# Kernel tuning notes

Hardware: AMD Instinct MI355X
Metric: run time of the kernel (lower is better)

Reference implementation:

```python
import jax, jax.numpy as jnp
import numpy as np

N = 200_000      # nodes
E = 6_400_000    # edges (avg degree 32)
ATT = 16         # scorer hidden dim
MAXD = 512       # mixer max_depth
C = 1.0          # curvature
EPS = 1e-15


def _mobius_add(a, b, c):
    # Mobius addition on the Poincare ball: a (+)_c b
    ab = jnp.sum(a * b, axis=-1, keepdims=True)
    aa = jnp.sum(a * a, axis=-1, keepdims=True)
    bb = jnp.sum(b * b, axis=-1, keepdims=True)
    num = (1.0 + 2.0 * c * ab + c * bb) * a + (1.0 - c * aa) * b
    den = 1.0 + 2.0 * c * ab + (c * c) * aa * bb
    return num / jnp.maximum(den, EPS)


def setup_inputs() -> dict:
    key = jax.random.key(0)
    ks = jax.random.split(key, 8)
    x = jax.random.normal(ks[0], (N, 2), dtype=jnp.float32)
    # keep nodes strictly inside the unit Poincare disk (|x| < 0.5)
    x = 0.5 * x / (1.0 + jnp.linalg.norm(x, axis=-1, keepdims=True))
    edge_index = jax.random.randint(ks[1], (2, E), 0, N, dtype=jnp.int32)
    depth = jax.random.randint(ks[2], (N,), 0, MAXD, dtype=jnp.int32)
    W1 = jax.random.normal(ks[3], (2, ATT), dtype=jnp.float32) * (1.0 / np.sqrt(2.0))
    b1 = jnp.zeros((ATT,), dtype=jnp.float32)
    W2 = jax.random.normal(ks[4], (ATT, 1), dtype=jnp.float32) * (1.0 / np.sqrt(ATT))
    eta = jnp.array(1.0, dtype=jnp.float32)
    depth_scale = 1.0 + 0.1 * jax.random.normal(ks[5], (MAXD, 1), dtype=jnp.float32)
    depth_theta = 0.1 * jax.random.normal(ks[6], (MAXD, 1), dtype=jnp.float32)
    return dict(x=x, edge_index=edge_index, depth=depth, W1=W1, b1=b1, W2=W2,
                eta=eta, depth_scale=depth_scale, depth_theta=depth_theta)


def reference(x, edge_index, depth, W1, b1, W2, eta, depth_scale, depth_theta):
    c = C
    sc = jnp.sqrt(jnp.asarray(c, dtype=x.dtype))
    row, col = edge_index[0], edge_index[1]
    xi = x[row]   # [E,2] target node of each edge
    xj = x[col]   # [E,2] source node of each edge

    # log_{xi}(xj): tangent vector at xi
    u = _mobius_add(-xi, xj, c)                                        # [E,2]
    un = jnp.maximum(jnp.linalg.norm(u, axis=-1, keepdims=True), EPS)  # [E,1]
    lam_i = 2.0 / jnp.maximum(1.0 - c * jnp.sum(xi * xi, axis=-1, keepdims=True), EPS)
    v = (2.0 / (sc * lam_i)) * jnp.arctanh(jnp.minimum(sc * un, 1.0 - 1e-5)) * (u / un)

    # tiny MLP attention score per edge
    h = jax.nn.gelu(v @ W1 + b1, approximate=False)   # [E,ATT]
    scores = (h @ W2)[:, 0]                           # [E]

    # segment softmax over edges grouped by target node `row`
    smax = jax.ops.segment_max(scores, row, num_segments=N)
    ex = jnp.exp(scores - smax[row])
    denom = jax.ops.segment_sum(ex, row, num_segments=N)
    alpha = ex / jnp.maximum(denom[row], 1e-15)       # [E]

    # weighted scatter-add of tangent vectors
    m = jax.ops.segment_sum(alpha[:, None] * v, row, num_segments=N)   # [N,2]

    # depth-gated rotation/scale in the tangent space (mixer)
    d = jnp.clip(depth, 0, MAXD - 1)
    k = depth_scale[d]            # [N,1]
    ang = depth_theta[d][:, 0]    # [N]
    ca, sa = jnp.cos(ang), jnp.sin(ang)
    m = k * jnp.stack([ca * m[:, 0] - sa * m[:, 1],
                       sa * m[:, 0] + ca * m[:, 1]], axis=-1)

    # exp_{x}(eta * m)
    w = eta * m
    wn = jnp.maximum(jnp.linalg.norm(w, axis=-1, keepdims=True), EPS)
    lam_x = 2.0 / jnp.maximum(1.0 - c * jnp.sum(x * x, axis=-1, keepdims=True), EPS)
    second = jnp.tanh(sc * lam_x * wn / 2.0) * (w / (sc * wn))
    return _mobius_add(x, second, c)
```

## Files before the change

### kernel.cpp

```cpp
#include <hip/hip_runtime.h>
#include <hip/hip_fp16.h>
#include <math.h>

#define EPSF 1e-15f
#define BSH  8
#define BSZ  (1 << BSH)
#define BMSK (BSZ - 1)
#define CAPB 9216
#define MAXNB 1024
#define AGG_T 1024
#define KSL   9
#define BIN_T 1024
#define LCH   4096

#define TBL   128
#define TW    129
#define TWSZ  (TW * TW)
#define VMIN  (-1.2f)
#define VH    (2.4f / 128.0f)
#define INVH  (128.0f / 2.4f)

__device__ __forceinline__ float fast_rcp(float x)  { return __builtin_amdgcn_rcpf(x); }
__device__ __forceinline__ float fast_rsq(float x)  { return __builtin_amdgcn_rsqf(x); }
__device__ __forceinline__ float fast_exp(float x)  { return __builtin_amdgcn_exp2f(x * 1.4426950408889634f); }

__device__ __forceinline__ unsigned int float_to_ordered(float f) {
    unsigned int u = __float_as_uint(f);
    return (u & 0x80000000u) ? ~u : (u | 0x80000000u);
}
__device__ __forceinline__ float ordered_to_float(unsigned int u) {
    u = (u & 0x80000000u) ? (u & 0x7FFFFFFFu) : ~u;
    return __uint_as_float(u);
}

__device__ __forceinline__ void edge_v_fast(float2 xi, float2 xj, float& vx, float& vy) {
    float ab = -(xi.x * xj.x + xi.y * xj.y);
    float aa = xi.x * xi.x + xi.y * xi.y;
    float bb = xj.x * xj.x + xj.y * xj.y;
    float f1 = 1.0f + 2.0f * ab + bb;
    float f2 = 1.0f - aa;
    float ux = f1 * (-xi.x) + f2 * xj.x;
    float uy = f1 * (-xi.y) + f2 * xj.y;
    float den = 1.0f + 2.0f * ab + aa * bb;
    float inv_den = fast_rcp(fmaxf(den, EPSF));
    ux *= inv_den; uy *= inv_den;
    float un2 = fmaxf(ux * ux + uy * uy, 1e-24f);
    float inv_un = fast_rsq(un2);
    float un = fminf(un2 * inv_un, 1.0f - 1e-5f);
    float t = 0.34657359027997264f * __builtin_amdgcn_logf((1.0f + un) * fast_rcp(1.0f - un));
    float s = fmaxf(f2, EPSF) * t * inv_un;
    vx = s * ux; vy = s * uy;
}

__device__ __forceinline__ void edge_v(float2 xi, float2 xj, float& vx, float& vy) {
    float ab = -(xi.x * xj.x + xi.y * xj.y);
    float aa = xi.x * xi.x + xi.y * xi.y;
    float bb = xj.x * xj.x + xj.y * xj.y;
    float f1 = 1.0f + 2.0f * ab + bb;
    float f2 = 1.0f - aa;
    float ux = f1 * (-xi.x) + f2 * xj.x;
    float uy = f1 * (-xi.y) + f2 * xj.y;
    float den = 1.0f + 2.0f * ab + aa * bb;
    float inv_den = 1.0f / fmaxf(den, EPSF);
    ux *= inv_den; uy *= inv_den;
    float un = fmaxf(sqrtf(ux * ux + uy * uy), EPSF);
    float t  = atanhf(fminf(un, 1.0f - 1e-5f));
    float s = fmaxf(f2, EPSF) * t / un;
    vx = s * ux; vy = s * uy;
}

__device__ __forceinline__ float edge_score(float vx, float vy,
                                            const float* __restrict__ W1,
                                            const float* __restrict__ b1,
                                            const float* __restrict__ W2) {
    float score = 0.0f;
#pragma unroll
    for (int k = 0; k < 16; ++k) {
        float z = fmaf(vx, W1[k], fmaf(vy, W1[16 + k], b1[k]));
        float g = 0.5f * z * (1.0f + erff(z * 0.70710678118654752f));
        score = fmaf(g, W2[k], score);
    }
    return score;
}

__device__ __forceinline__ float2 finalize_node(float2 xv, float mx, float my,
                                                int d, float eta,
                                                const float* __restrict__ dscale,
                                                const float* __restrict__ dtheta) {
    d = d < 0 ? 0 : (d > 511 ? 511 : d);
    float k   = dscale[d];
    float ang = dtheta[d];
    float ca = cosf(ang), sa = sinf(ang);
    float m0 = k * (ca * mx - sa * my);
    float m1 = k * (sa * mx + ca * my);

    float wx = eta * m0, wy = eta * m1;
    float wn = fmaxf(sqrtf(wx * wx + wy * wy), 1e-15f);

    float aa = xv.x * xv.x + xv.y * xv.y;
    float lam = 2.0f / fmaxf(1.0f - aa, 1e-15f);
    float fac = tanhf(lam * wn * 0.5f) / wn;
    float sx = fac * wx, sy = fac * wy;

    float ab = xv.x * sx + xv.y * sy;
    float bb = sx * sx + sy * sy;
    float n1 = 1.0f + 2.0f * ab + bb;
    float n2 = 1.0f - aa;
    float ox = n1 * xv.x + n2 * sx;
    float oy = n1 * xv.y + n2 * sy;
    float dd = 1.0f + 2.0f * ab + aa * bb;
    float inv = 1.0f / fmaxf(dd, 1e-15f);
    return make_float2(ox * inv, oy * inv);
}


__global__ void build_score_table(const float* __restrict__ W1,
                                  const float* __restrict__ b1,
                                  const float* __restrict__ W2,
                                  float* __restrict__ tbl) {
    int i = blockIdx.x * blockDim.x + threadIdx.x;
    if (i >= TWSZ) return;
    int iy = i / TW, ix = i - iy * TW;
    float vx = VMIN + VH * (float)ix;
    float vy = VMIN + VH * (float)iy;
    tbl[i] = edge_score(vx, vy, W1, b1, W2);
}

__global__ __launch_bounds__(BIN_T, 8)
void bin_edges(const int* __restrict__ ei,
               unsigned* __restrict__ cursor,
               unsigned* __restrict__ sorted,
               int E, int NB, int buildTbl,
               const float* __restrict__ W1,
               const float* __restrict__ b1,
               const float* __restrict__ W2,
               float* __restrict__ tbl) {
    __shared__ __align__(16) unsigned bkrank[LCH];
    __shared__ __align__(16) unsigned payload[LCH];
    __shared__ unsigned sortedLoc[LCH];
    __shared__ unsigned gdst[LCH];
    __shared__ unsigned hist[MAXNB];
    __shared__ unsigned loc[MAXNB];
    __shared__ unsigned gbase[MAXNB];
    __shared__ unsigned waveSum[16];

    int tid = threadIdx.x;

    if (buildTbl) {
        int gi = blockIdx.x * BIN_T + tid;
        if (gi < TWSZ) {
            int iy = gi / TW, ix = gi - iy * TW;
            float vx = VMIN + VH * (float)ix;
            float vy = VMIN + VH * (float)iy;
            tbl[gi] = edge_score(vx, vy, W1, b1, W2);
        }
    }

    int e0 = blockIdx.x * LCH;
    int cnt = min(E - e0, LCH);
    if (cnt <= 0) return;

    hist[tid] = 0;
    __syncthreads();

    if (((E | cnt) & 3) == 0) {
        int idx = tid << 2;
        if (idx < cnt) {
            const int4 r4 = *(const int4*)(ei + e0 + idx);
            const int4 c4 = *(const int4*)(ei + E + e0 + idx);
            unsigned bk0 = (unsigned)r4.x >> BSH; unsigned rk0 = atomicAdd(&hist[bk0], 1u);
            unsigned bk1 = (unsigned)r4.y >> BSH; unsigned rk1 = atomicAdd(&hist[bk1], 1u);
            unsigned bk2 = (unsigned)r4.z >> BSH; unsigned rk2 = atomicAdd(&hist[bk2], 1u);
            unsigned bk3 = (unsigned)r4.w >> BSH; unsigned rk3 = atomicAdd(&hist[bk3], 1u);
            *(uint4*)(bkrank + idx) = make_uint4((bk0 << 14) | rk0, (bk1 << 14) | rk1,
                                                 (bk2 << 14) | rk2, (bk3 << 14) | rk3);
            uint4 pl;
            pl.x = ((unsigned)(r4.x & BMSK) << 24) | (unsigned)c4.x;
            pl.y = ((unsigned)(r4.y & BMSK) << 24) | (unsigned)c4.y;
            pl.z = ((unsigned)(r4.z & BMSK) << 24) | (unsigned)c4.z;
            pl.w = ((unsigned)(r4.w & BMSK) << 24) | (unsigned)c4.w;
            *(uint4*)(payload + idx) = pl;
        }
    } else {
        for (int idx = tid; idx < cnt; idx += BIN_T) {
            int r = ei[e0 + idx];
            int c = ei[E + e0 + idx];
            unsigned bk = (unsigned)r >> BSH;
            unsigned rank = atomicAdd(&hist[bk], 1u);
            bkrank[idx] = (bk << 14) | rank;
            payload[idx] = ((unsigned)(r & BMSK) << 24) | (unsigned)c;
        }
    }
    __syncthreads();

    unsigned h = hist[tid];
    unsigned v = h;
    int lane = tid & 63;
    int wv = tid >> 6;
#pragma unroll
    for (int s = 1; s < 64; s <<= 1) {
        unsigned t = __shfl_up(v, s, 64);
        if (lane >= s) v += t;
    }
    if (lane == 63) waveSum[wv] = v;
    __syncthreads();
    if (wv == 0) {
        unsigned w2 = (lane < 16) ? waveSum[lane] : 0u;
#pragma unroll
        for (int s = 1; s < 16; s <<= 1) {
            unsigned t = __shfl_up(w2, s, 64);
            if (lane >= s) w2 += t;
        }
        if (lane < 16) waveSum[lane] = w2;
    }
    __syncthreads();
    unsigned base = wv ? waveSum[wv - 1] : 0u;
    loc[tid] = base + v - h;

    gbase[tid] = h ? atomicAdd(&cursor[tid], h) : 0u;
    __syncthreads();

    for (int idx = tid; idx < cnt; idx += BIN_T) {
        unsigned w = bkrank[idx];
        unsigned pos = loc[w >> 14] + (w & 0x3FFFu);
        sortedLoc[pos] = payload[idx];
        gdst[pos] = w;
    }
    __syncthreads();

    for (int idx = tid; idx < cnt; idx += BIN_T) {
        unsigned w = gdst[idx];
        unsigned bk = w >> 14;
        unsigned rel = gbase[bk] + (w & 0x3FFFu);
        if (rel < (unsigned)CAPB) sorted[bk * (unsigned)CAPB + rel] = sortedLoc[idx];
    }
}

__global__ __launch_bounds__(AGG_T, 8)
void aggregate(const float2* __restrict__ x,
               const unsigned* __restrict__ cursor,
               const unsigned* __restrict__ sorted,
               const int* __restrict__ depth,
               const float* __restrict__ tbl,
               const float* __restrict__ etaPtr,
               const float* __restrict__ dscale,
               const float* __restrict__ dtheta,
               float2* __restrict__ out, int N) {
    __shared__ float tl[TWSZ];
    __shared__ float2 xr[BSZ];
    __shared__ unsigned nmax[BSZ];
    __shared__ unsigned long long accP[BSZ];

    int b = blockIdx.x;
    int tid = threadIdx.x;
    int nb0 = b << BSH;
    int nodeCnt = min(BSZ, N - nb0);

    const unsigned* __restrict__ sb = sorted + (unsigned)b * CAPB;

    unsigned u[KSL];
    {
        uint4 ua = *(const uint4*)(sb + 4 * tid);
        uint4 ub = *(const uint4*)(sb + 4096 + 4 * tid);
        unsigned uc = sb[8192 + tid];
        u[0] = ua.x; u[1] = ua.y; u[2] = ua.z; u[3] = ua.w;
        u[4] = ub.x; u[5] = ub.y; u[6] = ub.z; u[7] = ub.w;
        u[8] = uc;
    }
    __builtin_amdgcn_sched_barrier(0);

    for (int i = tid; i < TWSZ; i += AGG_T) tl[i] = tbl[i];
    if (tid < BSZ) {
        nmax[tid] = 0u;
        accP[tid] = 0ull;
        if (tid < nodeCnt) xr[tid] = x[nb0 + tid];
    }

    unsigned cnt = cursor[b];
    cnt = cnt > (unsigned)CAPB ? (unsigned)CAPB : cnt;

#define SLOT(k) ((k) < 4 ? (unsigned)(4 * tid + (k)) \
               : (k) < 8 ? (unsigned)(4096 + 4 * tid + ((k) - 4)) \
                         : (unsigned)(8192 + tid))

    float2 xj[KSL];
#pragma unroll
    for (int k = 0; k < KSL; ++k) {
        unsigned i = SLOT(k);
        int c = (i < cnt) ? (int)(u[k] & 0xFFFFFFu) : 0;
        xj[k] = x[c];
    }
    __builtin_amdgcn_sched_barrier(0);
    __syncthreads();

    unsigned pkA[KSL];
    unsigned pkV[KSL];
#pragma unroll
    for (int k = 0; k < KSL; ++k) {
        unsigned i = SLOT(k);
        bool act = i < cnt;
        int rl = (int)(u[k] >> 24);
        float2 xi = xr[rl];
        float vx, vy;
        edge_v_fast(xi, xj[k], vx, vy);

        float tx = fminf(fmaxf((vx - VMIN) * INVH, 0.0f), 127.999f);
        float ty = fminf(fmaxf((vy - VMIN) * INVH, 0.0f), 127.999f);
        int ix = (int)tx, iy = (int)ty;
        float fx = tx - (float)ix, fy = ty - (float)iy;
        const float* row = tl + iy * TW + ix;
        float s00 = row[0], s01 = row[1];
        float s10 = row[TW], s11 = row[TW + 1];
        float sA = fmaf(fx, s01 - s00, s00);
        float sB = fmaf(fx, s11 - s10, s10);
        float score = fmaf(fy, sB - sA, sA);

        __half hs = __float2half_rn(score);
        float sq = __half2float(hs);
        unsigned short s16 = *(unsigned short*)&hs;
        __half2 h2 = __floats2half2_rn(vx, vy);
        pkA[k] = ((unsigned)rl << 16) | (unsigned)s16;
        pkV[k] = *(unsigned*)&h2;
        if (act) atomicMax(&nmax[rl], float_to_ordered(sq));
    }
    __syncthreads();

#pragma unroll
    for (int k = 0; k < KSL; ++k) {
        unsigned i = SLOT(k);
        if (i >= cnt) continue;
        int rlk = (int)(pkA[k] >> 16);
        unsigned short s16 = (unsigned short)(pkA[k] & 0xFFFFu);
        __half hs = *(__half*)&s16;
        float s = __half2float(hs);
        float mxs = ordered_to_float(nmax[rlk]);
        float ex = fast_exp(s - mxs);
        __half2 h2 = *(__half2*)&pkV[k];
        float2 v2 = __half22float2(h2);
        unsigned e0 = __float2uint_rn(ex * 16384.0f);
        unsigned e1 = __float2uint_rn(ex * (v2.x + 2.0f) * 0.25f * 16384.0f);
        unsigned e2 = __float2uint_rn(ex * (v2.y + 2.0f) * 0.25f * 16384.0f);
        unsigned long long pk = (unsigned long long)e0
                              | ((unsigned long long)e1 << 21)
                              | ((unsigned long long)e2 << 42);
        atomicAdd(&accP[rlk], pk);
    }
#undef SLOT
    __syncthreads();

    if (tid >= nodeCnt) return;
    unsigned long long w = accP[tid];
    float F0 = (float)(unsigned int)(w & 0x1FFFFFull);
    float F1 = (float)(unsigned int)((w >> 21) & 0x1FFFFFull);
    float F2 = (float)(unsigned int)(w >> 42);
    float mx = 0.0f, my = 0.0f;
    if (F0 > 0.0f) {
        float inv = 1.0f / F0;
        mx = 4.0f * F1 * inv - 2.0f;
        my = 4.0f * F2 * inv - 2.0f;
    }
    int i = nb0 + tid;
    out[i] = finalize_node(xr[tid], mx, my, depth[i], etaPtr[0], dscale, dtheta);
}


__global__ void init_kernel(unsigned int* __restrict__ smax,
                            unsigned long long* __restrict__ maccP, int N) {
    int i = blockIdx.x * blockDim.x + threadIdx.x;
    if (i < N) {
        smax[i] = float_to_ordered(-INFINITY);
        maccP[i] = 0ull;
    }
}

__global__ void pass1_score_max(const float2* __restrict__ x,
                                const int* __restrict__ ei,
                                const float* __restrict__ W1,
                                const float* __restrict__ b1,
                                const float* __restrict__ W2,
                                unsigned int* __restrict__ smax, int E) {
    int e = blockIdx.x * blockDim.x + threadIdx.x;
    if (e >= E) return;
    int r = ei[e];
    int c = ei[E + e];
    float vx, vy;
    edge_v(x[r], x[c], vx, vy);
    float score = edge_score(vx, vy, W1, b1, W2);
    atomicMax(&smax[r], float_to_ordered(score));
}

#define PK_SCALE 16384.0f

__global__ void pass2_accum(const float2* __restrict__ x,
                            const int* __restrict__ ei,
                            const float* __restrict__ W1,
                            const float* __restrict__ b1,
                            const float* __restrict__ W2,
                            const unsigned int* __restrict__ smax,
                            unsigned long long* __restrict__ maccP, int E) {
    int e = blockIdx.x * blockDim.x + threadIdx.x;
    if (e >= E) return;
    int r = ei[e];
    int c = ei[E + e];
    float vx, vy;
    edge_v(x[r], x[c], vx, vy);
    float score = edge_score(vx, vy, W1, b1, W2);
    float mx = ordered_to_float(smax[r]);
    float ex = expf(score - mx);
    unsigned e0 = __float2uint_rn(ex * PK_SCALE);
    unsigned e1 = __float2uint_rn(ex * (vx + 2.0f) * 0.25f * PK_SCALE);
    unsigned e2 = __float2uint_rn(ex * (vy + 2.0f) * 0.25f * PK_SCALE);
    unsigned long long pk = (unsigned long long)e0
                          | ((unsigned long long)e1 << 21)
                          | ((unsigned long long)e2 << 42);
    atomicAdd(&maccP[r], pk);
}

__global__ void pass3_finalize(const float2* __restrict__ x,
                               const int* __restrict__ depth,
                               const unsigned long long* __restrict__ maccP,
                               const float* __restrict__ etaPtr,
                               const float* __restrict__ dscale,
                               const float* __restrict__ dtheta,
                               float2* __restrict__ out, int N) {
    int i = blockIdx.x * blockDim.x + threadIdx.x;
    if (i >= N) return;
    unsigned long long w = maccP[i];
    float F0 = (float)(unsigned int)(w & 0x1FFFFFull);
    float F1 = (float)(unsigned int)((w >> 21) & 0x1FFFFFull);
    float F2 = (float)(unsigned int)(w >> 42);
    float mx = 0.0f, my = 0.0f;
    if (F0 > 0.0f) {
        float inv = 1.0f / F0;
        mx = 4.0f * F1 * inv - 2.0f;
        my = 4.0f * F2 * inv - 2.0f;
    }
    out[i] = finalize_node(x[i], mx, my, depth[i], etaPtr[0], dscale, dtheta);
}


extern "C" void kernel_launch(void* const* d_in, const int* in_sizes, int n_in,
                              void* d_out, int out_size, void* d_ws, size_t ws_size,
                              hipStream_t stream) {
    const float2* x   = (const float2*)d_in[0];
    const int* ei     = (const int*)d_in[1];
    const int* depth  = (const int*)d_in[2];
    const float* W1   = (const float*)d_in[3];
    const float* b1   = (const float*)d_in[4];
    const float* W2   = (const float*)d_in[5];
    const float* eta  = (const float*)d_in[6];
    const float* dsc  = (const float*)d_in[7];
    const float* dth  = (const float*)d_in[8];
    float2* out = (float2*)d_out;

    int N = in_sizes[0] / 2;
    int E = in_sizes[1] / 2;
    int NB = (N + BSZ - 1) >> BSH;

    const int B = 256;
    size_t sortedBytes = (size_t)NB * CAPB * 4;
    size_t need = 4096 + sortedBytes + (size_t)TWSZ * 4;
    if (NB <= MAXNB && ws_size >= need) {
        unsigned* cursor = (unsigned*)d_ws;
        unsigned* sorted = (unsigned*)((char*)d_ws + 4096);
        float* tbl = (float*)((char*)d_ws + 4096 + sortedBytes);
        int binG = (E + LCH - 1) / LCH;
        int tblBlocks = (TWSZ + BIN_T - 1) / BIN_T;
        int buildInBin = (binG >= tblBlocks) ? 1 : 0;
        hipMemsetAsync(cursor, 0, (size_t)NB * sizeof(unsigned), stream);
        if (!buildInBin)
            build_score_table<<<(TWSZ + B - 1) / B, B, 0, stream>>>(W1, b1, W2, tbl);
        bin_edges<<<binG, BIN_T, 0, stream>>>(ei, cursor, sorted, E, NB, buildInBin,
                                              W1, b1, W2, tbl);
        aggregate<<<NB, AGG_T, 0, stream>>>(x, cursor, sorted, depth, tbl,
                                            eta, dsc, dth, out, N);
    } else {
        unsigned long long* maccP = (unsigned long long*)d_ws;
        unsigned int* smax = (unsigned int*)(maccP + N);
        init_kernel<<<(N + B - 1) / B, B, 0, stream>>>(smax, maccP, N);
        pass1_score_max<<<(E + B - 1) / B, B, 0, stream>>>(x, ei, W1, b1, W2, smax, E);
        pass2_accum<<<(E + B - 1) / B, B, 0, stream>>>(x, ei, W1, b1, W2, smax, maccP, E);
        pass3_finalize<<<(N + B - 1) / B, B, 0, stream>>>(x, depth, maccP, eta, dsc, dth, out, N);
    }
}
```

Before: 180.7 us.

## Use global table max as softmax shift to drop per-node max pass

Computes the global maximum of the precomputed score table while building it, and uses that constant as the softmax shift in the aggregate kernel instead of a per-node segment max. This removes the shared-memory atomicMax pass, one block barrier, and the half-precision and fixed-point packing, replacing them with three fp32 shared atomics per edge. It also vectorizes the table copy into shared memory with float4 loads. The risk is underflow of exp for nodes whose scores are far below the global max, and more shared atomics per edge.

```diff
diff --git a/kernel.cpp b/kernel.cpp
--- a/kernel.cpp
+++ b/kernel.cpp
@@ -16,6 +16,7 @@
 #define TBL   128
 #define TW    129
 #define TWSZ  (TW * TW)
+#define TW4   ((TWSZ) / 4)
 #define VMIN  (-1.2f)
 #define VH    (2.4f / 128.0f)
 #define INVH  (128.0f / 2.4f)
@@ -117,13 +118,16 @@
 __global__ void build_score_table(const float* __restrict__ W1,
                                   const float* __restrict__ b1,
                                   const float* __restrict__ W2,
-                                  float* __restrict__ tbl) {
+                                  float* __restrict__ tbl,
+                                  unsigned* __restrict__ tblMaxSlot) {
     int i = blockIdx.x * blockDim.x + threadIdx.x;
     if (i >= TWSZ) return;
     int iy = i / TW, ix = i - iy * TW;
     float vx = VMIN + VH * (float)ix;
     float vy = VMIN + VH * (float)iy;
-    tbl[i] = edge_score(vx, vy, W1, b1, W2);
+    float v = edge_score(vx, vy, W1, b1, W2);
+    tbl[i] = v;
+    atomicMax(tblMaxSlot, float_to_ordered(v));
 }
 
 __global__ __launch_bounds__(BIN_T, 8)
@@ -152,7 +156,9 @@
             int iy = gi / TW, ix = gi - iy * TW;
             float vx = VMIN + VH * (float)ix;
             float vy = VMIN + VH * (float)iy;
-            tbl[gi] = edge_score(vx, vy, W1, b1, W2);
+            float v = edge_score(vx, vy, W1, b1, W2);
+            tbl[gi] = v;
+            atomicMax(&cursor[MAXNB - 1], float_to_ordered(v));
         }
     }
 
@@ -246,10 +252,9 @@
                const float* __restrict__ dscale,
                const float* __restrict__ dtheta,
                float2* __restrict__ out, int N) {
-    __shared__ float tl[TWSZ];
+    __shared__ __align__(16) float tl[TWSZ];
     __shared__ float2 xr[BSZ];
-    __shared__ unsigned nmax[BSZ];
-    __shared__ unsigned long long accP[BSZ];
+    __shared__ float accF[3 * BSZ];
 
     int b = blockIdx.x;
     int tid = threadIdx.x;
@@ -269,13 +274,23 @@
     }
     __builtin_amdgcn_sched_barrier(0);
 
-    for (int i = tid; i < TWSZ; i += AGG_T) tl[i] = tbl[i];
-    if (tid < BSZ) {
-        nmax[tid] = 0u;
-        accP[tid] = 0ull;
-        if (tid < nodeCnt) xr[tid] = x[nb0 + tid];
-    }
-
+    {
+        const float4* t4 = (const float4*)tbl;
+        float4* tl4 = (float4*)tl;
+#pragma unroll
+        for (int k = 0; k < 4; ++k) {
+            int i = tid + k * AGG_T;
+            tl4[i] = t4[i];
+        }
+        int i5 = tid + 4 * AGG_T;
+        if (i5 < TW4) tl4[i5] = t4[i5];
+        if (tid == 0) tl[TWSZ - 1] = tbl[TWSZ - 1];
+    }
+    if (tid < BSZ) xr[tid] = (tid < nodeCnt) ? x[nb0 + tid] : make_float2(0.0f, 0.0f);
+    if (tid < 3 * BSZ) accF[tid] = 0.0f;
+
+    float tblMax = ordered_to_float(cursor[MAXNB - 1]);
+    if (!(tblMax > -1e30f && tblMax < 1e30f)) tblMax = 0.0f;
     unsigned cnt = cursor[b];
     cnt = cnt > (unsigned)CAPB ? (unsigned)CAPB : cnt;
 
@@ -293,12 +308,11 @@
     __builtin_amdgcn_sched_barrier(0);
     __syncthreads();
 
-    unsigned pkA[KSL];
-    unsigned pkV[KSL];
 #pragma unroll
     for (int k = 0; k < KSL; ++k) {
         unsigned i = SLOT(k);
         bool act = i < cnt;
+        if (k == 8 && !act) continue;
         int rl = (int)(u[k] >> 24);
         float2 xi = xr[rl];
         float vx, vy;
@@ -315,49 +329,25 @@
         float sB = fmaf(fx, s11 - s10, s10);
         float score = fmaf(fy, sB - sA, sA);
 
-        __half hs = __float2half_rn(score);
-        float sq = __half2float(hs);
-        unsigned short s16 = *(unsigned short*)&hs;
-        __half2 h2 = __floats2half2_rn(vx, vy);
-        pkA[k] = ((unsigned)rl << 16) | (unsigned)s16;
-        pkV[k] = *(unsigned*)&h2;
-        if (act) atomicMax(&nmax[rl], float_to_ordered(sq));
-    }
-    __syncthreads();
-
-#pragma unroll
-    for (int k = 0; k < KSL; ++k) {
-        unsigned i = SLOT(k);
-        if (i >= cnt) continue;
-        int rlk = (int)(pkA[k] >> 16);
-        unsigned short s16 = (unsigned short)(pkA[k] & 0xFFFFu);
-        __half hs = *(__half*)&s16;
-        float s = __half2float(hs);
-        float mxs = ordered_to_float(nmax[rlk]);
-        float ex = fast_exp(s - mxs);
-        __half2 h2 = *(__half2*)&pkV[k];
-        float2 v2 = __half22float2(h2);
-        unsigned e0 = __float2uint_rn(ex * 16384.0f);
-        unsigned e1 = __float2uint_rn(ex * (v2.x + 2.0f) * 0.25f * 16384.0f);
-        unsigned e2 = __float2uint_rn(ex * (v2.y + 2.0f) * 0.25f * 16384.0f);
-        unsigned long long pk = (unsigned long long)e0
-                              | ((unsigned long long)e1 << 21)
-                              | ((unsigned long long)e2 << 42);
-        atomicAdd(&accP[rlk], pk);
+        float ex = fast_exp(score - tblMax);
+        if (act) {
+            atomicAdd(&accF[3 * rl + 0], ex);
+            atomicAdd(&accF[3 * rl + 1], ex * vx);
+            atomicAdd(&accF[3 * rl + 2], ex * vy);
+        }
     }
 #undef SLOT
     __syncthreads();
 
     if (tid >= nodeCnt) return;
-    unsigned long long w = accP[tid];
-    float F0 = (float)(unsigned int)(w & 0x1FFFFFull);
-    float F1 = (float)(unsigned int)((w >> 21) & 0x1FFFFFull);
-    float F2 = (float)(unsigned int)(w >> 42);
+    float F0 = accF[3 * tid + 0];
+    float F1 = accF[3 * tid + 1];
+    float F2 = accF[3 * tid + 2];
     float mx = 0.0f, my = 0.0f;
     if (F0 > 0.0f) {
         float inv = 1.0f / F0;
-        mx = 4.0f * F1 * inv - 2.0f;
-        my = 4.0f * F2 * inv - 2.0f;
+        mx = F1 * inv;
+        my = F2 * inv;
     }
     int i = nb0 + tid;
     out[i] = finalize_node(xr[tid], mx, my, depth[i], etaPtr[0], dscale, dtheta);
@@ -460,16 +450,17 @@
     const int B = 256;
     size_t sortedBytes = (size_t)NB * CAPB * 4;
     size_t need = 4096 + sortedBytes + (size_t)TWSZ * 4;
-    if (NB <= MAXNB && ws_size >= need) {
+    if (NB <= MAXNB - 1 && ws_size >= need) {
         unsigned* cursor = (unsigned*)d_ws;
         unsigned* sorted = (unsigned*)((char*)d_ws + 4096);
         float* tbl = (float*)((char*)d_ws + 4096 + sortedBytes);
         int binG = (E + LCH - 1) / LCH;
         int tblBlocks = (TWSZ + BIN_T - 1) / BIN_T;
         int buildInBin = (binG >= tblBlocks) ? 1 : 0;
-        hipMemsetAsync(cursor, 0, (size_t)NB * sizeof(unsigned), stream);
+        hipMemsetAsync(cursor, 0, (size_t)MAXNB * sizeof(unsigned), stream);
         if (!buildInBin)
-            build_score_table<<<(TWSZ + B - 1) / B, B, 0, stream>>>(W1, b1, W2, tbl);
+            build_score_table<<<(TWSZ + B - 1) / B, B, 0, stream>>>(W1, b1, W2, tbl,
+                                                                    &cursor[MAXNB - 1]);
         bin_edges<<<binG, BIN_T, 0, stream>>>(ei, cursor, sorted, E, NB, buildInBin,
                                               W1, b1, W2, tbl);
         aggregate<<<NB, AGG_T, 0, stream>>>(x, cursor, sorted, depth, tbl,
```

Measured after the change: 282.0 us. +56.0%, slower.
